# Kernel tuning notes

Measured on AMD Instinct MI355X. Metric: run time of the kernel, lower is better.

## Reference

```python
import jax, jax.numpy as jnp
import numpy as np

D_EMBED = 1024
D_QUERY = 512
NEG_INF = -1.0e9  # matches masked_fill value in the torch module


def setup_inputs() -> dict:
    key = jax.random.key(0)
    k_x, k_q, k_k, k_v, k_m = jax.random.split(key, 5)
    B, T = 8, 2048
    x = jax.random.normal(k_x, (B, T, D_EMBED), dtype=jnp.float32)
    # nn.Linear(d_embed, d_query, bias=False): y = x @ W^T; store W as (d_embed, d_query)
    sc = 1.0 / np.sqrt(D_EMBED)
    Wq = jax.random.normal(k_q, (D_EMBED, D_QUERY), dtype=jnp.float32) * sc
    Wk = jax.random.normal(k_k, (D_EMBED, D_QUERY), dtype=jnp.float32) * sc
    Wv = jax.random.normal(k_v, (D_EMBED, D_QUERY), dtype=jnp.float32) * sc
    attn_mask = jax.random.randint(k_m, (B, T), 0, 2).astype(jnp.bool_)
    return {"x": x, "Wq": Wq, "Wk": Wk, "Wv": Wv, "attn_mask": attn_mask}


def reference(x, Wq, Wk, Wv, attn_mask):
    # x: (B, T, d_embed)
    q = jnp.einsum("btd,dq->btq", x, Wq)  # (B, T, d_query)
    k = jnp.einsum("btd,dq->btq", x, Wk)
    v = jnp.einsum("btd,dq->btq", x, Wv)
    # NOTE: original module applies NO 1/sqrt(d) scaling.
    logits = jnp.einsum("btq,bsq->bts", q, k)  # (B, T, T)
    # attn_mask (B, T) broadcasts over the query axis: mask keys where mask is False
    logits = jnp.where(attn_mask[..., None, :], logits, NEG_INF)
    A = jax.nn.softmax(logits, axis=-1)
    return jnp.einsum("bts,bsq->btq", A, v)  # (B, T, d_query)
```

## Files before the change

kernel.cpp:

```cpp
#include <hip/hip_runtime.h>
#include <hip/hip_bf16.h>
#include <cstddef>
#include <cstdint>

#define BATCH 8
#define SEQ   2048
#define DEMB  1024
#define DQ    512

typedef __attribute__((ext_vector_type(8))) _Float16 f16x8;
typedef __attribute__((ext_vector_type(4))) float f32x4;

#define MFMA16(a, b, c) __builtin_amdgcn_mfma_f32_16x16x32_f16((a), (b), (c), 0, 0, 0)

#define GLDS16(gp, lp) __builtin_amdgcn_global_load_lds(                      \
    (const __attribute__((address_space(1))) void*)(gp),                      \
    (__attribute__((address_space(3))) void*)(lp), 16, 0, 0)

#define VM_BAR(N)                                                             \
  asm volatile("s_waitcnt vmcnt(" #N ")\n\ts_barrier" ::: "memory")
#define VM_LGKM_BAR(N)                                                        \
  asm volatile("s_waitcnt vmcnt(" #N ") lgkmcnt(0)\n\ts_barrier" ::: "memory")

__global__ __launch_bounds__(256) void prep_all(
    const float* __restrict__ x, _Float16* __restrict__ xh,
    const float* __restrict__ Wq, const float* __restrict__ Wk,
    const float* __restrict__ Wv, _Float16* __restrict__ wt,
    const int* __restrict__ maskg, int* __restrict__ pidx,
    int* __restrict__ cnt)
{
  const int bid = blockIdx.x;
  const int tid = threadIdx.x;

  if (bid < 8192) {
    size_t i = ((size_t)bid * 256 + tid) * 8;
    float4 a = *(const float4*)&x[i];
    float4 b = *(const float4*)&x[i + 4];
    f16x8 h;
    h[0] = (_Float16)a.x; h[1] = (_Float16)a.y;
    h[2] = (_Float16)a.z; h[3] = (_Float16)a.w;
    h[4] = (_Float16)b.x; h[5] = (_Float16)b.y;
    h[6] = (_Float16)b.z; h[7] = (_Float16)b.w;
    *(f16x8*)&xh[i] = h;
  } else if (bid < 9728) {
    int qidx = (bid - 8192) * 256 + tid;
    int w   = qidx >> 17;
    int rem = qidx & 131071;
    int k   = rem >> 7;
    int n   = (rem & 127) * 4;
    const float* W = (w == 0) ? Wq : (w == 1) ? Wk : Wv;
    float4 v = *(const float4*)&W[(size_t)k * DQ + n];
    _Float16* dst = wt + (size_t)w * (DQ * DEMB);
    dst[(size_t)(n + 0) * DEMB + k] = (_Float16)v.x;
    dst[(size_t)(n + 1) * DEMB + k] = (_Float16)v.y;
    dst[(size_t)(n + 2) * DEMB + k] = (_Float16)v.z;
    dst[(size_t)(n + 3) * DEMB + k] = (_Float16)v.w;
  } else {
    const int b = bid - 9728;
    __shared__ int tsum[256];
    int mv[8], s = 0;
    #pragma unroll
    for (int j = 0; j < 8; j++) {
      mv[j] = maskg[b * SEQ + tid * 8 + j];
      s += mv[j];
    }
    tsum[tid] = s;
    __syncthreads();
    for (int d = 1; d < 256; d <<= 1) {
      int v = (tid >= d) ? tsum[tid - d] : 0;
      __syncthreads();
      tsum[tid] += v;
      __syncthreads();
    }
    if (tid == 255) cnt[b] = tsum[255];
    int run = tsum[tid] - s;
    #pragma unroll
    for (int j = 0; j < 8; j++) {
      pidx[b * SEQ + tid * 8 + j] = mv[j] ? run : -1;
      run += mv[j];
    }
  }
}

__global__ __launch_bounds__(512) void proj_f16(
    const _Float16* __restrict__ xh, const _Float16* __restrict__ wt,
    const int* __restrict__ pidx,
    _Float16* __restrict__ kf, _Float16* __restrict__ vt,
    _Float16* __restrict__ qpack)
{
  const int w  = blockIdx.z;
  const int mt = blockIdx.y, nt = blockIdx.x;

  __shared__ _Float16 Xs[128][40];
  __shared__ _Float16 Ws[256][40];

  const int tid  = threadIdx.x;
  const int wave = tid >> 6, l = tid & 63;
  const int wm = wave >> 2;
  const int wn = wave & 3;
  const int lo4 = l & 15, hi2 = l >> 4;

  f32x4 acc[4][4];
  #pragma unroll
  for (int mf = 0; mf < 4; mf++)
    #pragma unroll
    for (int nf = 0; nf < 4; nf++)
      #pragma unroll
      for (int i = 0; i < 4; i++) acc[mf][nf][i] = 0.f;

  const int    xsrow = tid >> 2;
  const int    xskh  = (tid & 3) * 8;
  const size_t xbase = (size_t)(mt * 128 + xsrow) * DEMB + xskh;
  const int    wsrow = tid >> 1;
  const int    wskh  = (tid & 1) * 16;
  const size_t wbase = (size_t)w * (DQ * DEMB)
                     + (size_t)(nt * 256 + wsrow) * DEMB + wskh;

  #pragma unroll 1
  for (int k0 = 0; k0 < DEMB; k0 += 32) {
    *(f16x8*)&Xs[xsrow][xskh]    = *(const f16x8*)&xh[xbase + k0];
    *(f16x8*)&Ws[wsrow][wskh]    = *(const f16x8*)&wt[wbase + k0];
    *(f16x8*)&Ws[wsrow][wskh+8]  = *(const f16x8*)&wt[wbase + k0 + 8];
    __syncthreads();

    f16x8 a[4], bfr[4];
    #pragma unroll
    for (int mf = 0; mf < 4; mf++)
      a[mf] = *(const f16x8*)&Xs[wm*64 + mf*16 + lo4][hi2*8];
    #pragma unroll
    for (int nf = 0; nf < 4; nf++)
      bfr[nf] = *(const f16x8*)&Ws[wn*64 + nf*16 + lo4][hi2*8];
    #pragma unroll
    for (int mf = 0; mf < 4; mf++)
      #pragma unroll
      for (int nf = 0; nf < 4; nf++)
        acc[mf][nf] = MFMA16(a[mf], bfr[nf], acc[mf][nf]);
    __syncthreads();
  }

  const int mb = mt * 128 + wm * 64;
  const int nb = nt * 256 + wn * 64;
  #pragma unroll
  for (int mf = 0; mf < 4; mf++)
    #pragma unroll
    for (int nf = 0; nf < 4; nf++)
      #pragma unroll
      for (int i = 0; i < 4; i++) {
        int m = mb + mf*16 + hi2*4 + i;
        int n = nb + nf*16 + lo4;
        float val = acc[mf][nf][i];
        if (w == 0) {
          _Float16 h  = (_Float16)val;
          _Float16 lo = (_Float16)(val - (float)h);
          size_t base = (size_t)(m >> 6) * 65536 + (size_t)(m & 63) * 512 + n;
          qpack[base]         = h;
          qpack[base + 32768] = lo;
        } else if (w == 1) {
          int d_ = pidx[m];
          if (d_ >= 0)
            kf[((size_t)((m >> 11) << 11) + d_) * 512 + n] = (_Float16)val;
        } else {
          int d_ = pidx[m];
          if (d_ >= 0)
            vt[(size_t)(m >> 11) * (512 * 2048) + (size_t)n * 2048 + d_]
                = (_Float16)val;
        }
      }
}

__global__ __launch_bounds__(512, 2) void flash_v4(
    const _Float16* __restrict__ kfp, const _Float16* __restrict__ vtp,
    const int* __restrict__ cntg,
    float* dout)
{
  const int bb = blockIdx.x & 7;
  const int qt = blockIdx.x >> 3;
  const int q0 = qt * 64;

  const int tid = threadIdx.x;
  const int w = tid >> 6, l = tid & 63;
  const int qw = w & 3;
  const int kw = w >> 2;
  const int lo4 = l & 15, hi2 = l >> 4;

  __shared__ _Float16 Kst[2][64][256];
  __shared__ _Float16 Vst[2][256][64];
  __shared__ _Float16 P[64 * 64];
  __shared__ float pmax[2][64], psum[2][64];

  const _Float16* qpk = (const _Float16*)dout + (size_t)(bb * 32 + qt) * 65536;
  const char*     kb  = (const char*)(kfp + (size_t)bb * SEQ * 512);
  const char*     vtb = (const char*)(vtp + (size_t)bb * (512 * 2048));

  const _Float16* qhi = qpk + (size_t)(qw * 16 + lo4) * 512;
  const _Float16* qlo = qhi + 32768;

  const int cnt = cntg[bb];
  const int nkt = (cnt + 63) >> 6;

#define STAGE_K(KT, H, B) do {                                                \
    const char* kg_ = kb + (size_t)(KT) * 64 * 1024;                          \
    char* lb_ = (char*)&Kst[(B)][0][0];                                       \
    _Pragma("unroll")                                                         \
    for (int i_ = 0; i_ < 4; i_++) {                                          \
      int D_ = i_ * 8192 + tid * 16;                                          \
      int row_ = D_ >> 9, cb_ = D_ & 511;                                     \
      GLDS16(kg_ + (size_t)row_ * 1024 + (H) * 512 +                          \
                 (cb_ ^ ((row_ & 7) << 4)),                                   \
             lb_ + D_);                                                       \
    } } while (0)

#define STAGE_V(KT, H, B) do {                                                \
    const char* vg_ = vtb + (size_t)(KT) * 128;                               \
    char* lb_ = (char*)&Vst[(B)][0][0];                                       \
    _Pragma("unroll")                                                         \
    for (int i_ = 0; i_ < 4; i_++) {                                          \
      int D_ = i_ * 8192 + tid * 16;                                          \
      int row_ = D_ >> 7, cb_ = D_ & 127;                                     \
      GLDS16(vg_ + (size_t)((H) * 256 + row_) * 4096 +                        \
                 (cb_ ^ ((row_ & 7) << 4)),                                   \
             lb_ + D_);                                                       \
    } } while (0)

#define QK_HALF(H, B) do {                                                    \
    const char* kl_ = (const char*)&Kst[(B)][0][0];                           \
    const int r0_ = kw * 32 + lo4, r1_ = r0_ + 16;                            \
    const int sw_ = (lo4 & 7) << 4;                                           \
    _Pragma("unroll")                                                         \
    for (int s_ = 0; s_ < 8; s_++) {                                          \
      const int dby_ = (s_ * 32 + hi2 * 8) * 2;                               \
      f16x8 k0 = *(const f16x8*)(kl_ + r0_ * 512 + (dby_ ^ sw_));             \
      f16x8 k1 = *(const f16x8*)(kl_ + r1_ * 512 + (dby_ ^ sw_));             \
      __builtin_amdgcn_s_setprio(1);                                          \
      S[0] = MFMA16(fq[(H) * 8 + s_], k0, S[0]);                              \
      S[1] = MFMA16(fq[(H) * 8 + s_], k1, S[1]);                              \
      S[0] = MFMA16(fql[(H) * 8 + s_], k0, S[0]);                             \
      S[1] = MFMA16(fql[(H) * 8 + s_], k1, S[1]);                             \
      __builtin_amdgcn_s_setprio(0);                                          \
    } } while (0)

#define PV_HALF(H, B) do {                                                    \
    const char* vl_ = (const char*)&Vst[(B)][0][0];                           \
    _Pragma("unroll")                                                         \
    for (int j_ = 0; j_ < 8; j_++) {                                          \
      const int dl_ = j_ * 32 + kw * 16 + lo4;                                \
      const int vs_ = (dl_ & 7) << 4;                                         \
      f16x8 v0 = *(const f16x8*)(vl_ + dl_ * 128 + ((hi2 * 16) ^ vs_));       \
      f16x8 v1 = *(const f16x8*)(vl_ + dl_ * 128 + ((64 + hi2 * 16) ^ vs_));  \
      __builtin_amdgcn_s_setprio(1);                                          \
      o[(H) * 8 + j_] = MFMA16(pa[0], v0, o[(H) * 8 + j_]);                   \
      o[(H) * 8 + j_] = MFMA16(pa[1], v1, o[(H) * 8 + j_]);                   \
      __builtin_amdgcn_s_setprio(0);                                          \
    } } while (0)

  f16x8 fq[16], fql[16];
  #pragma unroll
  for (int st = 0; st < 16; st++) {
    fq[st]  = *(const f16x8*)(qhi + st * 32 + hi2 * 8);
    fql[st] = *(const f16x8*)(qlo + st * 32 + hi2 * 8);
  }
  STAGE_K(0, 0, 0);
  __syncthreads();

  f32x4 o[16];
  #pragma unroll
  for (int f = 0; f < 16; f++)
    #pragma unroll
    for (int i = 0; i < 4; i++) o[f][i] = 0.f;

  float m_run[4], l_run[4], m_runP = -3.0e38f;
  #pragma unroll
  for (int i = 0; i < 4; i++) { m_run[i] = -3.0e38f; l_run[i] = 0.f; }

  const int ki0 = kw * 32 + lo4;
  const int ki1 = ki0 + 16;

  #pragma unroll 1
  for (int kt = 0; kt < nkt; kt++) {
    const int key0 = kt * 64;

    STAGE_K(kt, 1, 1);
    STAGE_V(kt, 0, 0);
    VM_BAR(8);

    f32x4 S[2];
    #pragma unroll
    for (int f = 0; f < 2; f++)
      #pragma unroll
      for (int i = 0; i < 4; i++) S[f][i] = 0.f;
    QK_HALF(0, 0);

    VM_BAR(4);
    QK_HALF(1, 1);

    STAGE_V(kt, 1, 1);
    STAGE_K(kt + 1, 0, 0);

    const bool t0 = (key0 + ki0 >= cnt);
    const bool t1 = (key0 + ki1 >= cnt);
    #pragma unroll
    for (int i = 0; i < 4; i++) {
      if (t0) S[0][i] = -1.0e9f;
      if (t1) S[1][i] = -1.0e9f;
      float mx = fmaxf(S[0][i], S[1][i]);
      #pragma unroll
      for (int off = 1; off < 16; off <<= 1)
        mx = fmaxf(mx, __shfl_xor(mx, off, 64));
      float p0 = __expf(S[0][i] - mx);
      float p1 = __expf(S[1][i] - mx);
      int row = qw*16 + hi2*4 + i;
      int swz = (row & 7) << 4;
      int b0  = (row*128 + (kw*32 + lo4)*2) ^ swz;
      int b1  = (row*128 + (kw*32 + 16 + lo4)*2) ^ swz;
      *(_Float16*)((char*)P + b0) = (_Float16)p0;
      *(_Float16*)((char*)P + b1) = (_Float16)p1;
      float ps = p0 + p1;
      #pragma unroll
      for (int off = 1; off < 16; off <<= 1) ps += __shfl_xor(ps, off, 64);
      if (lo4 == 0) { pmax[kw][row] = mx; psum[kw][row] = ps; }
    }

    VM_LGKM_BAR(8);

    float oscale[4];
    #pragma unroll
    for (int i = 0; i < 4; i++) {
      int row = qw*16 + hi2*4 + i;
      float m0 = pmax[0][row], m1 = pmax[1][row];
      float s0 = psum[0][row], s1 = psum[1][row];
      float mn = fmaxf(m_run[i], fmaxf(m0, m1));
      oscale[i] = __expf(m_run[i] - mn);
      l_run[i] = l_run[i] * oscale[i]
               + __expf(m0 - mn) * s0 + __expf(m1 - mn) * s1;
      m_run[i] = mn;
    }
    #pragma unroll
    for (int f = 0; f < 16; f++)
      #pragma unroll
      for (int i = 0; i < 4; i++) o[f][i] *= oscale[i];

    f16x8 pa[2];
    {
      const int prow = qw*16 + lo4;
      float m0p = pmax[0][prow], m1p = pmax[1][prow];
      float mnp = fmaxf(m_runP, fmaxf(m0p, m1p));
      m_runP = mnp;
      _Float16 c0 = (_Float16)__expf(m0p - mnp);
      _Float16 c1 = (_Float16)__expf(m1p - mnp);
      const int psw = (prow & 7) << 4;
      pa[0] = *(const f16x8*)((const char*)P + prow*128 + ((hi2*16) ^ psw));
      pa[1] = *(const f16x8*)((const char*)P + prow*128 + ((64 + hi2*16) ^ psw));
      pa[0] = pa[0] * c0;
      pa[1] = pa[1] * c1;
    }

    PV_HALF(0, 0);
    VM_BAR(4);
    PV_HALF(1, 1);
  }
#undef STAGE_K
#undef STAGE_V
#undef QK_HALF
#undef PV_HALF

  asm volatile("s_waitcnt vmcnt(0)" ::: "memory");

  #pragma unroll
  for (int i = 0; i < 4; i++) {
    float inv = 1.0f / l_run[i];
    int rowg = bb * SEQ + q0 + qw*16 + hi2*4 + i;
    #pragma unroll
    for (int h = 0; h < 2; h++)
      #pragma unroll
      for (int j = 0; j < 8; j++) {
        int d = h*256 + j*32 + kw*16 + lo4;
        dout[(size_t)rowg * 512 + d] = o[h*8 + j][i] * inv;
      }
  }
}

extern "C" void kernel_launch(void* const* d_in, const int* in_sizes, int n_in,
                              void* d_out, int out_size, void* d_ws, size_t ws_size,
                              hipStream_t stream)
{
  const float* x    = (const float*)d_in[0];
  const float* Wq   = (const float*)d_in[1];
  const float* Wk   = (const float*)d_in[2];
  const float* Wv   = (const float*)d_in[3];
  const int*   mask = (const int*)d_in[4];

  _Float16* wsh = (_Float16*)d_ws;
  _Float16* KF = wsh;
  _Float16* VT = wsh +  8388608;
  _Float16* WT = wsh + 16777216;
  _Float16* XH = wsh + 18350080;
  int* PIDX    = (int*)(wsh + 35127296);
  int* CNT     = PIDX + 16384;

  prep_all<<<9736, 256, 0, stream>>>(x, XH, Wq, Wk, Wv, WT, mask, PIDX, CNT);

  dim3 pgrid(2, 128, 3);
  proj_f16<<<pgrid, 512, 0, stream>>>(XH, WT, PIDX, KF, VT, (_Float16*)d_out);

  flash_v4<<<256, 512, 0, stream>>>(KF, VT, CNT, (float*)d_out);
}
```

Before: 256.3 us.

## Software-pipeline flash loop: overlap PV of previous tile with QK of current

Restructures the flash attention main loop so the P·V product for key tile kt-1 is interleaved with the Q·K product for tile kt. P is double-buffered in LDS, the merge/rescale step moves to the start of the next iteration, and an epilogue drains the last tile. Staging is reordered to load V and K halves for the first tile up front, with a prologue and different wait points. The aim is to hide softmax and barrier latency behind MFMA work, at the cost of more LDS, more live registers and a more intricate set of buffer reuse hazards.

```diff
diff --git a/kernel.cpp b/kernel.cpp
--- a/kernel.cpp
+++ b/kernel.cpp
@@ -21,6 +21,8 @@
   asm volatile("s_waitcnt vmcnt(" #N ")\n\ts_barrier" ::: "memory")
 #define VM_LGKM_BAR(N)                                                        \
   asm volatile("s_waitcnt vmcnt(" #N ") lgkmcnt(0)\n\ts_barrier" ::: "memory")
+#define BAR()                                                                 \
+  asm volatile("s_barrier" ::: "memory")
 
 __global__ __launch_bounds__(256) void prep_all(
     const float* __restrict__ x, _Float16* __restrict__ xh,
@@ -168,7 +170,7 @@
       }
 }
 
-__global__ __launch_bounds__(512, 2) void flash_v4(
+__global__ __launch_bounds__(512, 2) void flash_v7(
     const _Float16* __restrict__ kfp, const _Float16* __restrict__ vtp,
     const int* __restrict__ cntg,
     float* dout)
@@ -185,7 +187,7 @@
 
   __shared__ _Float16 Kst[2][64][256];
   __shared__ _Float16 Vst[2][256][64];
-  __shared__ _Float16 P[64 * 64];
+  __shared__ _Float16 P[2][64 * 64];
   __shared__ float pmax[2][64], psum[2][64];
 
   const _Float16* qpk = (const _Float16*)dout + (size_t)(bb * 32 + qt) * 65536;
@@ -253,13 +255,48 @@
       __builtin_amdgcn_s_setprio(0);                                          \
     } } while (0)
 
+#define MERGE_PA(PB) do {                                                     \
+    float oscale[4];                                                          \
+    _Pragma("unroll")                                                         \
+    for (int i = 0; i < 4; i++) {                                             \
+      int row = qw*16 + hi2*4 + i;                                            \
+      float m0 = pmax[0][row], m1 = pmax[1][row];                             \
+      float s0 = psum[0][row], s1 = psum[1][row];                             \
+      float mn = fmaxf(m_run[i], fmaxf(m0, m1));                              \
+      oscale[i] = __expf(m_run[i] - mn);                                      \
+      l_run[i] = l_run[i] * oscale[i]                                         \
+               + __expf(m0 - mn) * s0 + __expf(m1 - mn) * s1;                 \
+      m_run[i] = mn;                                                          \
+    }                                                                         \
+    _Pragma("unroll")                                                         \
+    for (int f = 0; f < 16; f++)                                              \
+      _Pragma("unroll")                                                       \
+      for (int i = 0; i < 4; i++) o[f][i] *= oscale[i];                       \
+    {                                                                         \
+      const int prow = qw*16 + lo4;                                           \
+      float m0p = pmax[0][prow], m1p = pmax[1][prow];                         \
+      float mnp = fmaxf(m_runP, fmaxf(m0p, m1p));                             \
+      m_runP = mnp;                                                           \
+      _Float16 c0 = (_Float16)__expf(m0p - mnp);                              \
+      _Float16 c1 = (_Float16)__expf(m1p - mnp);                              \
+      const int psw = (prow & 7) << 4;                                        \
+      const char* pb_ = (const char*)&P[(PB)][0];                             \
+      pa[0] = *(const f16x8*)(pb_ + prow*128 + ((hi2*16) ^ psw));             \
+      pa[1] = *(const f16x8*)(pb_ + prow*128 + ((64 + hi2*16) ^ psw));        \
+      pa[0] = pa[0] * c0;                                                     \
+      pa[1] = pa[1] * c1;                                                     \
+    } } while (0)
+
   f16x8 fq[16], fql[16];
   #pragma unroll
   for (int st = 0; st < 16; st++) {
     fq[st]  = *(const f16x8*)(qhi + st * 32 + hi2 * 8);
     fql[st] = *(const f16x8*)(qlo + st * 32 + hi2 * 8);
   }
+  STAGE_V(0, 0, 0);
   STAGE_K(0, 0, 0);
+  STAGE_V(0, 1, 1);
+  STAGE_K(0, 1, 1);
   __syncthreads();
 
   f32x4 o[16];
@@ -278,22 +315,28 @@
   #pragma unroll 1
   for (int kt = 0; kt < nkt; kt++) {
     const int key0 = kt * 64;
-
-    STAGE_K(kt, 1, 1);
+    const int cur = kt & 1;
+
+    VM_LGKM_BAR(8);
+
+    f32x4 S[2];
+    #pragma unroll
+    for (int f = 0; f < 2; f++)
+      #pragma unroll
+      for (int i = 0; i < 4; i++) S[f][i] = 0.f;
+
+    f16x8 pa[2];
+    if (kt) MERGE_PA(cur ^ 1);
+
+    QK_HALF(0, 0);
+    if (kt) PV_HALF(0, 0);
+
+    VM_BAR(0);
+
+    QK_HALF(1, 1);
+    if (kt) PV_HALF(1, 1);
+
     STAGE_V(kt, 0, 0);
-    VM_BAR(8);
-
-    f32x4 S[2];
-    #pragma unroll
-    for (int f = 0; f < 2; f++)
-      #pragma unroll
-      for (int i = 0; i < 4; i++) S[f][i] = 0.f;
-    QK_HALF(0, 0);
-
-    VM_BAR(4);
-    QK_HALF(1, 1);
-
-    STAGE_V(kt, 1, 1);
     STAGE_K(kt + 1, 0, 0);
 
     const bool t0 = (key0 + ki0 >= cnt);
@@ -312,58 +355,31 @@
       int swz = (row & 7) << 4;
       int b0  = (row*128 + (kw*32 + lo4)*2) ^ swz;
       int b1  = (row*128 + (kw*32 + 16 + lo4)*2) ^ swz;
-      *(_Float16*)((char*)P + b0) = (_Float16)p0;
-      *(_Float16*)((char*)P + b1) = (_Float16)p1;
+      *(_Float16*)((char*)&P[cur][0] + b0) = (_Float16)p0;
+      *(_Float16*)((char*)&P[cur][0] + b1) = (_Float16)p1;
       float ps = p0 + p1;
       #pragma unroll
       for (int off = 1; off < 16; off <<= 1) ps += __shfl_xor(ps, off, 64);
       if (lo4 == 0) { pmax[kw][row] = mx; psum[kw][row] = ps; }
     }
 
-    VM_LGKM_BAR(8);
-
-    float oscale[4];
-    #pragma unroll
-    for (int i = 0; i < 4; i++) {
-      int row = qw*16 + hi2*4 + i;
-      float m0 = pmax[0][row], m1 = pmax[1][row];
-      float s0 = psum[0][row], s1 = psum[1][row];
-      float mn = fmaxf(m_run[i], fmaxf(m0, m1));
-      oscale[i] = __expf(m_run[i] - mn);
-      l_run[i] = l_run[i] * oscale[i]
-               + __expf(m0 - mn) * s0 + __expf(m1 - mn) * s1;
-      m_run[i] = mn;
-    }
-    #pragma unroll
-    for (int f = 0; f < 16; f++)
-      #pragma unroll
-      for (int i = 0; i < 4; i++) o[f][i] *= oscale[i];
-
-    f16x8 pa[2];
-    {
-      const int prow = qw*16 + lo4;
-      float m0p = pmax[0][prow], m1p = pmax[1][prow];
-      float mnp = fmaxf(m_runP, fmaxf(m0p, m1p));
-      m_runP = mnp;
-      _Float16 c0 = (_Float16)__expf(m0p - mnp);
-      _Float16 c1 = (_Float16)__expf(m1p - mnp);
-      const int psw = (prow & 7) << 4;
-      pa[0] = *(const f16x8*)((const char*)P + prow*128 + ((hi2*16) ^ psw));
-      pa[1] = *(const f16x8*)((const char*)P + prow*128 + ((64 + hi2*16) ^ psw));
-      pa[0] = pa[0] * c0;
-      pa[1] = pa[1] * c1;
-    }
-
-    PV_HALF(0, 0);
-    VM_BAR(4);
-    PV_HALF(1, 1);
+    BAR();
+    STAGE_V(kt, 1, 1);
+    STAGE_K(kt + 1, 1, 1);
   }
 #undef STAGE_K
 #undef STAGE_V
 #undef QK_HALF
+
+  asm volatile("s_waitcnt vmcnt(0) lgkmcnt(0)\n\ts_barrier" ::: "memory");
+  {
+    f16x8 pa[2];
+    MERGE_PA((nkt - 1) & 1);
+    PV_HALF(0, 0);
+    PV_HALF(1, 1);
+  }
 #undef PV_HALF
-
-  asm volatile("s_waitcnt vmcnt(0)" ::: "memory");
+#undef MERGE_PA
 
   #pragma unroll
   for (int i = 0; i < 4; i++) {
@@ -402,5 +418,5 @@
   dim3 pgrid(2, 128, 3);
   proj_f16<<<pgrid, 512, 0, stream>>>(XH, WT, PIDX, KF, VT, (_Float16*)d_out);
 
-  flash_v4<<<256, 512, 0, stream>>>(KF, VT, CNT, (float*)d_out);
+  flash_v7<<<256, 512, 0, stream>>>(KF, VT, CNT, (float*)d_out);
 }
```

New measurement: 254.5 us. Within noise of the previous version (-0.7%).
